# Performance work log

Measured on AMD Instinct MI355X. Metric: run time of the kernel, lower is better.

## Reference

```python
import jax, jax.numpy as jnp
import numpy as np

B, N, FD, H = 8, 256, 1024, 256
RATIO, TEMP = 0.6, 0.5


def setup_inputs() -> dict:
    key = jax.random.key(0)
    ks = jax.random.split(key, 5)
    x = jax.random.normal(ks[0], (B, N, FD), dtype=jnp.float32)
    s1 = 1.0 / np.sqrt(2 * FD)
    W1 = jax.random.uniform(ks[1], (H, 2 * FD), minval=-s1, maxval=s1, dtype=jnp.float32)
    b1 = jax.random.uniform(ks[2], (H,), minval=-s1, maxval=s1, dtype=jnp.float32)
    s2 = 1.0 / np.sqrt(H)
    W2 = jax.random.uniform(ks[3], (1, H), minval=-s2, maxval=s2, dtype=jnp.float32)
    b2 = jax.random.uniform(ks[4], (1,), minval=-s2, maxval=s2, dtype=jnp.float32)
    return {"x": x, "W1": W1, "b1": b1, "W2": W2, "b2": b2}


def reference(x, W1, b1, W2, b2):
    Bb, Nn, Fd = x.shape
    # Linear on cat([row, col]) == row @ W1[:, :F].T + col @ W1[:, F:].T + b1,
    # so project nodes once and broadcast-add instead of materializing [N,N,2F].
    pr = jnp.einsum('bnf,hf->bnh', x, W1[:, :Fd])  # row projections
    pc = jnp.einsum('bnf,hf->bnh', x, W1[:, Fd:])  # col projections
    h = jax.nn.relu(pr[:, :, None, :] + pc[:, None, :, :] + b1)  # [B,N,N,H]
    edge_scores = jnp.einsum('bijh,h->bij', h, W2[0]) + b2[0]    # [B,N,N]
    flat = edge_scores.reshape(Bb, Nn * Nn)
    soft_mask = jax.nn.softmax(flat / TEMP, axis=1)
    k = int(RATIO * Nn * Nn)
    topk_vals, _ = jax.lax.top_k(soft_mask, k)
    threshold = topk_vals[:, -1:]
    causal_mask = jnp.where(soft_mask >= threshold, soft_mask, jnp.zeros_like(soft_mask))
    causal_mask = causal_mask / (causal_mask.sum(axis=1, keepdims=True) + 1e-12)
    conf_mask = 1.0 - causal_mask
    causal_adj = causal_mask.reshape(Bb, Nn, Nn)
    conf_adj = conf_mask.reshape(Bb, Nn, Nn)
    return (causal_adj, conf_adj, edge_scores, soft_mask)
```

## Files before the change

### kernel.cpp

```cpp
#include <hip/hip_runtime.h>

#define BB 8
#define NN 256
#define FDIM 1024
#define HDIM 256
#define NSQ 65536
#define ROWS 2048
#define KSEL 39321
#define NBIN 16384

typedef short s16x8 __attribute__((ext_vector_type(8)));
typedef float f32x4 __attribute__((ext_vector_type(4)));

__device__ __forceinline__ unsigned fkey(float f) {
  unsigned u = __float_as_uint(f);
  return (u & 0x80000000u) ? ~u : (u | 0x80000000u);
}
__device__ __forceinline__ float finv(unsigned k) {
  unsigned u = (k & 0x80000000u) ? (k & 0x7fffffffu) : ~k;
  return __uint_as_float(u);
}
__device__ __forceinline__ unsigned short f2bf(float f) {
  unsigned u = __float_as_uint(f);
  unsigned r = (u + 0x7fffu + ((u >> 16) & 1u)) >> 16;
  return (unsigned short)r;
}

__global__ __launch_bounds__(256) void k_prep(const float* __restrict__ X,
                                              const float* __restrict__ W1,
                                              unsigned short* __restrict__ XB,
                                              unsigned short* __restrict__ W1B,
                                              unsigned* __restrict__ zero) {
  const int bx = blockIdx.x, t = threadIdx.x;
  if (bx < 1280) {
    const float* src = (bx < 1024) ? X : W1;
    unsigned short* dst = (bx < 1024) ? XB : W1B;
    const int idx = ((bx < 1024 ? bx : bx - 1024) * 256 + t) * 8;
    float4 v0 = *(const float4*)&src[idx];
    float4 v1 = *(const float4*)&src[idx + 4];
    s16x8 o;
    o[0] = (short)f2bf(v0.x); o[1] = (short)f2bf(v0.y); o[2] = (short)f2bf(v0.z); o[3] = (short)f2bf(v0.w);
    o[4] = (short)f2bf(v1.x); o[5] = (short)f2bf(v1.y); o[6] = (short)f2bf(v1.z); o[7] = (short)f2bf(v1.w);
    *(s16x8*)&dst[idx] = o;
  } else {
    const int idx = ((bx - 1280) * 256 + t) * 4;
    *(uint4*)&zero[idx] = make_uint4(0u, 0u, 0u, 0u);
  }
}

#define LDSW 72
__global__ __launch_bounds__(256) void k_gemm(const unsigned short* __restrict__ XB,
                                              const unsigned short* __restrict__ W1B,
                                              const float* __restrict__ b1,
                                              float* __restrict__ PRBT,
                                              float* __restrict__ PCT) {
  const int bm = blockIdx.x * 64;
  const int bn = blockIdx.y * 64;
  const int t = threadIdx.x;
  __shared__ short As[64 * LDSW];
  __shared__ short Bs[64 * LDSW];
  const int sr = t >> 2, cg = t & 3;
  const unsigned short* pa = XB + (bm + sr) * FDIM + cg * 16;
  const unsigned short* pb = (bn < 256)
      ? (W1B + (bn + sr) * (2 * FDIM) + cg * 16)
      : (W1B + (bn - 256 + sr) * (2 * FDIM) + FDIM + cg * 16);
  const int w = t >> 6, lane = t & 63;
  const int wm = (w >> 1) * 32, wn = (w & 1) * 32;
  const int q = lane >> 4, m16 = lane & 15;
  f32x4 acc[2][2] = {};
  for (int k0 = 0; k0 < FDIM; k0 += 64) {
    s16x8 a0 = *(const s16x8*)(pa + k0);
    s16x8 a1 = *(const s16x8*)(pa + k0 + 8);
    s16x8 b0 = *(const s16x8*)(pb + k0);
    s16x8 b1v = *(const s16x8*)(pb + k0 + 8);
    __syncthreads();
    *(s16x8*)&As[sr * LDSW + cg * 16]     = a0;
    *(s16x8*)&As[sr * LDSW + cg * 16 + 8] = a1;
    *(s16x8*)&Bs[sr * LDSW + cg * 16]     = b0;
    *(s16x8*)&Bs[sr * LDSW + cg * 16 + 8] = b1v;
    __syncthreads();
    {
      s16x8 af0 = *(s16x8*)&As[(wm + m16) * LDSW + q * 8];
      s16x8 af1 = *(s16x8*)&As[(wm + 16 + m16) * LDSW + q * 8];
      s16x8 bf0 = *(s16x8*)&Bs[(wn + m16) * LDSW + q * 8];
      s16x8 bf1 = *(s16x8*)&Bs[(wn + 16 + m16) * LDSW + q * 8];
      acc[0][0] = __builtin_amdgcn_mfma_f32_16x16x32_bf16(af0, bf0, acc[0][0], 0, 0, 0);
      acc[0][1] = __builtin_amdgcn_mfma_f32_16x16x32_bf16(af0, bf1, acc[0][1], 0, 0, 0);
      acc[1][0] = __builtin_amdgcn_mfma_f32_16x16x32_bf16(af1, bf0, acc[1][0], 0, 0, 0);
      acc[1][1] = __builtin_amdgcn_mfma_f32_16x16x32_bf16(af1, bf1, acc[1][1], 0, 0, 0);
    }
    {
      s16x8 af0 = *(s16x8*)&As[(wm + m16) * LDSW + 32 + q * 8];
      s16x8 af1 = *(s16x8*)&As[(wm + 16 + m16) * LDSW + 32 + q * 8];
      s16x8 bf0 = *(s16x8*)&Bs[(wn + m16) * LDSW + 32 + q * 8];
      s16x8 bf1 = *(s16x8*)&Bs[(wn + 16 + m16) * LDSW + 32 + q * 8];
      acc[0][0] = __builtin_amdgcn_mfma_f32_16x16x32_bf16(af0, bf0, acc[0][0], 0, 0, 0);
      acc[0][1] = __builtin_amdgcn_mfma_f32_16x16x32_bf16(af0, bf1, acc[0][1], 0, 0, 0);
      acc[1][0] = __builtin_amdgcn_mfma_f32_16x16x32_bf16(af1, bf0, acc[1][0], 0, 0, 0);
      acc[1][1] = __builtin_amdgcn_mfma_f32_16x16x32_bf16(af1, bf1, acc[1][1], 0, 0, 0);
    }
  }
#pragma unroll
  for (int rt = 0; rt < 2; ++rt) {
#pragma unroll
    for (int ct = 0; ct < 2; ++ct) {
      const int hn = bn + wn + ct * 16 + m16;
      const int row0 = bm + wm + rt * 16 + q * 4;
      if (hn < 256) {
        const float bias = b1[hn];
        float4 v = make_float4(acc[rt][ct][0] + bias, acc[rt][ct][1] + bias,
                               acc[rt][ct][2] + bias, acc[rt][ct][3] + bias);
        *(float4*)&PRBT[hn * ROWS + row0] = v;
      } else {
        float4 v = make_float4(acc[rt][ct][0], acc[rt][ct][1],
                               acc[rt][ct][2], acc[rt][ct][3]);
        *(float4*)&PCT[(hn - 256) * ROWS + row0] = v;
      }
    }
  }
}

__global__ __launch_bounds__(256) void k_edge(const float* __restrict__ PRBT,
                                              const float* __restrict__ PCT,
                                              const float* __restrict__ W2,
                                              const float* __restrict__ b2,
                                              float* __restrict__ edge,
                                              unsigned* __restrict__ gcount,
                                              float* __restrict__ gvsum) {
  const int b = blockIdx.z;
  const int i0 = blockIdx.y * 64, j0 = blockIdx.x * 32;
  const int t = threadIdx.x;
  __shared__ float prs[64][68];
  __shared__ float pcs[64][36];
  __shared__ float w2s[HDIM];
  __shared__ unsigned lhc[NBIN / 2];
  __shared__ float lhv[NBIN];
  w2s[t] = W2[t];
#pragma unroll
  for (int i = 0; i < 8; ++i) ((uint4*)lhc)[t + i * 256] = make_uint4(0u, 0u, 0u, 0u);
#pragma unroll
  for (int i = 0; i < 16; ++i) ((float4*)lhv)[t + i * 256] = make_float4(0.f, 0.f, 0.f, 0.f);
  const float bias = b2[0];
  const int tmi = t >> 4, tnj = t & 15;
  float acc[4][2] = {};
  for (int h0 = 0; h0 < HDIM; h0 += 64) {
    __syncthreads();
#pragma unroll
    for (int it = 0; it < 4; ++it) {
      int hh = it * 16 + (t >> 4);
      int ig = t & 15;
      *(float4*)&prs[hh][ig * 4] =
          *(const float4*)&PRBT[(h0 + hh) * ROWS + b * NN + i0 + ig * 4];
    }
#pragma unroll
    for (int it = 0; it < 2; ++it) {
      int hh = it * 32 + (t >> 3);
      int jg = t & 7;
      *(float4*)&pcs[hh][jg * 4] =
          *(const float4*)&PCT[(h0 + hh) * ROWS + b * NN + j0 + jg * 4];
    }
    __syncthreads();
#pragma unroll 8
    for (int h = 0; h < 64; ++h) {
      const float w = w2s[h0 + h];
      const float4 a = *(const float4*)&prs[h][tmi * 4];
      const float2 c = *(const float2*)&pcs[h][tnj * 2];
      const float ai[4] = {a.x, a.y, a.z, a.w};
#pragma unroll
      for (int i = 0; i < 4; ++i) {
        acc[i][0] += fmaxf(ai[i] + c.x, 0.f) * w;
        acc[i][1] += fmaxf(ai[i] + c.y, 0.f) * w;
      }
    }
  }
  const int ibase = i0 + tmi * 4, jbase = j0 + tnj * 2;
#pragma unroll
  for (int i = 0; i < 4; ++i) {
    float2 v = make_float2(acc[i][0] + bias, acc[i][1] + bias);
    *(float2*)&edge[b * NSQ + (ibase + i) * NN + jbase] = v;
    float ex = __expf(v.x * 2.f), ey = __expf(v.y * 2.f);
    unsigned bx = fkey(v.x) >> 18, by = fkey(v.y) >> 18;
    atomicAdd(&lhc[bx >> 1], 1u << ((bx & 1) * 16));
    atomicAdd(&lhv[bx], ex);
    atomicAdd(&lhc[by >> 1], 1u << ((by & 1) * 16));
    atomicAdd(&lhv[by], ey);
  }
  __syncthreads();
  unsigned* gc = gcount + b * NBIN;
  float* gv = gvsum + b * NBIN;
#pragma unroll
  for (int i = 0; i < 32; ++i) {
    const int idx = t + i * 256;
    unsigned wv = lhc[idx];
    if (wv) {
      unsigned lo = wv & 0xFFFFu, hi = wv >> 16;
      if (lo) atomicAdd(&gc[2 * idx], lo);
      if (hi) atomicAdd(&gc[2 * idx + 1], hi);
    }
  }
#pragma unroll
  for (int i = 0; i < 64; ++i) {
    const int idx = t + i * 256;
    float vv = lhv[idx];
    if (vv != 0.f) atomicAdd(&gv[idx], vv);
  }
}

__global__ __launch_bounds__(256) void k_out(const float* __restrict__ edge,
                                             const unsigned* __restrict__ gcount,
                                             const float* __restrict__ gvsum,
                                             float* __restrict__ soft,
                                             float* __restrict__ causal,
                                             float* __restrict__ conf) {
  const int b = blockIdx.y;
  const int t = threadIdx.x;
  __shared__ unsigned S[256];
  __shared__ float V[256];
  __shared__ unsigned ou[1];
  __shared__ float of[3];
  const unsigned* hc = gcount + b * NBIN;
  const float* hv = gvsum + b * NBIN;
  unsigned cs = 0; float vs = 0.f;
  for (int i = 0; i < 64; ++i) { cs += hc[t * 64 + i]; vs += hv[t * 64 + i]; }
  S[t] = cs; V[t] = vs;
  __syncthreads();
  for (int off = 1; off < 256; off <<= 1) {
    unsigned su = (t + off < 256) ? S[t + off] : 0u;
    float vu = (t + off < 256) ? V[t + off] : 0.f;
    __syncthreads();
    S[t] += su; V[t] += vu;
    __syncthreads();
  }
  if (t == 0) of[2] = V[0];
  const int above = (int)(S[t] - cs);
  if (above < KSEL && (int)S[t] >= KSEL) {
    int cum = above;
    float vcum = V[t] - vs;
    for (int i = 63; i >= 0; --i) {
      unsigned c = hc[t * 64 + i];
      float v = hv[t * 64 + i];
      cum += (int)c;
      if (cum >= KSEL) { ou[0] = (unsigned)(t * 64 + i); of[0] = vcum; of[1] = v; break; }
      vcum += v;
    }
  }
  __syncthreads();
  const float th = finv(ou[0] << 18);
  const float Z = of[2];
  const float invZ = 1.f / Z;
  const float msum = (of[0] + of[1]) * invZ;
  const float invD = 1.f / (msum + 1e-12f);
  const int off = b * NSQ + blockIdx.x * 2048 + t * 8;
#pragma unroll
  for (int i = 0; i < 8; i += 4) {
    float4 v = *(const float4*)&edge[off + i];
    float4 o = make_float4(__expf(v.x * 2.f) * invZ, __expf(v.y * 2.f) * invZ,
                           __expf(v.z * 2.f) * invZ, __expf(v.w * 2.f) * invZ);
    *(float4*)&soft[off + i] = o;
    float cx = v.x >= th ? o.x * invD : 0.f;
    float cy = v.y >= th ? o.y * invD : 0.f;
    float cz = v.z >= th ? o.z * invD : 0.f;
    float cw = v.w >= th ? o.w * invD : 0.f;
    *(float4*)&causal[off + i] = make_float4(cx, cy, cz, cw);
    *(float4*)&conf[off + i]   = make_float4(1.f - cx, 1.f - cy, 1.f - cz, 1.f - cw);
  }
}

extern "C" void kernel_launch(void* const* d_in, const int* in_sizes, int n_in,
                              void* d_out, int out_size, void* d_ws, size_t ws_size,
                              hipStream_t stream) {
  const float* x  = (const float*)d_in[0];
  const float* W1 = (const float*)d_in[1];
  const float* b1 = (const float*)d_in[2];
  const float* W2 = (const float*)d_in[3];
  const float* b2 = (const float*)d_in[4];

  float* out = (float*)d_out;
  float* causal = out;
  float* conf   = out + 1 * 524288;
  float* edge   = out + 2 * 524288;
  float* soft   = out + 3 * 524288;

  float* ws = (float*)d_ws;
  float*          PRBT   = ws;
  float*          PCT    = ws + 524288;
  unsigned short* XB     = (unsigned short*)(ws + 1048576);
  unsigned short* W1B    = (unsigned short*)(ws + 2097152);
  unsigned*       gcount = (unsigned*)(ws + 2359296);
  float*          gvsum  = (float*)(ws + 2490368);

  k_prep<<<1536, 256, 0, stream>>>(x, W1, XB, W1B, gcount);
  k_gemm<<<dim3(32, 8), 256, 0, stream>>>(XB, W1B, b1, PRBT, PCT);
  k_edge<<<dim3(8, 4, 8), 256, 0, stream>>>(PRBT, PCT, W2, b2, edge, gcount, gvsum);
  k_out<<<dim3(32, 8), 256, 0, stream>>>(edge, gcount, gvsum, soft, causal, conf);
}
```

Before: 120.4 us.

## Halve histogram bins, double k_edge threads, prefetch GEMM tiles in registers

The top-k histogram shrinks from 16384 to 8192 bins per batch by dropping one more mantissa bit from the sort key. This cuts the LDS footprint and the cost of zeroing and flushing the histogram in k_edge and of scanning it in k_out. k_edge now runs 512 threads per block, each computing a 2x2 output micro-tile instead of 4x2, so each of the 256 blocks has more waves to hide latency. The GEMM loads the next K-slice into registers before the current one is consumed. The risk is that the coarser bins make the top-k threshold cruder, so more elements near it could be misclassified.

```diff
diff --git a/kernel.cpp b/kernel.cpp
--- a/kernel.cpp
+++ b/kernel.cpp
@@ -7,7 +7,7 @@
 #define NSQ 65536
 #define ROWS 2048
 #define KSEL 39321
-#define NBIN 16384
+#define NBIN 8192
 
 typedef short s16x8 __attribute__((ext_vector_type(8)));
 typedef float f32x4 __attribute__((ext_vector_type(4)));
@@ -68,16 +68,22 @@
   const int wm = (w >> 1) * 32, wn = (w & 1) * 32;
   const int q = lane >> 4, m16 = lane & 15;
   f32x4 acc[2][2] = {};
+  s16x8 ra0 = *(const s16x8*)(pa);
+  s16x8 ra1 = *(const s16x8*)(pa + 8);
+  s16x8 rb0 = *(const s16x8*)(pb);
+  s16x8 rb1 = *(const s16x8*)(pb + 8);
   for (int k0 = 0; k0 < FDIM; k0 += 64) {
-    s16x8 a0 = *(const s16x8*)(pa + k0);
-    s16x8 a1 = *(const s16x8*)(pa + k0 + 8);
-    s16x8 b0 = *(const s16x8*)(pb + k0);
-    s16x8 b1v = *(const s16x8*)(pb + k0 + 8);
-    __syncthreads();
-    *(s16x8*)&As[sr * LDSW + cg * 16]     = a0;
-    *(s16x8*)&As[sr * LDSW + cg * 16 + 8] = a1;
-    *(s16x8*)&Bs[sr * LDSW + cg * 16]     = b0;
-    *(s16x8*)&Bs[sr * LDSW + cg * 16 + 8] = b1v;
+    __syncthreads();
+    *(s16x8*)&As[sr * LDSW + cg * 16]     = ra0;
+    *(s16x8*)&As[sr * LDSW + cg * 16 + 8] = ra1;
+    *(s16x8*)&Bs[sr * LDSW + cg * 16]     = rb0;
+    *(s16x8*)&Bs[sr * LDSW + cg * 16 + 8] = rb1;
+    if (k0 + 64 < FDIM) {
+      ra0 = *(const s16x8*)(pa + k0 + 64);
+      ra1 = *(const s16x8*)(pa + k0 + 72);
+      rb0 = *(const s16x8*)(pb + k0 + 64);
+      rb1 = *(const s16x8*)(pb + k0 + 72);
+    }
     __syncthreads();
     {
       s16x8 af0 = *(s16x8*)&As[(wm + m16) * LDSW + q * 8];
@@ -120,7 +126,7 @@
   }
 }
 
-__global__ __launch_bounds__(256) void k_edge(const float* __restrict__ PRBT,
+__global__ __launch_bounds__(512) void k_edge(const float* __restrict__ PRBT,
                                               const float* __restrict__ PCT,
                                               const float* __restrict__ W2,
                                               const float* __restrict__ b2,
@@ -135,27 +141,25 @@
   __shared__ float w2s[HDIM];
   __shared__ unsigned lhc[NBIN / 2];
   __shared__ float lhv[NBIN];
-  w2s[t] = W2[t];
-#pragma unroll
-  for (int i = 0; i < 8; ++i) ((uint4*)lhc)[t + i * 256] = make_uint4(0u, 0u, 0u, 0u);
-#pragma unroll
-  for (int i = 0; i < 16; ++i) ((float4*)lhv)[t + i * 256] = make_float4(0.f, 0.f, 0.f, 0.f);
+  if (t < HDIM) w2s[t] = W2[t];
+#pragma unroll
+  for (int i = 0; i < 2; ++i) ((uint4*)lhc)[t + i * 512] = make_uint4(0u, 0u, 0u, 0u);
+#pragma unroll
+  for (int i = 0; i < 4; ++i) ((float4*)lhv)[t + i * 512] = make_float4(0.f, 0.f, 0.f, 0.f);
   const float bias = b2[0];
   const int tmi = t >> 4, tnj = t & 15;
-  float acc[4][2] = {};
+  float acc[2][2] = {};
   for (int h0 = 0; h0 < HDIM; h0 += 64) {
     __syncthreads();
 #pragma unroll
-    for (int it = 0; it < 4; ++it) {
-      int hh = it * 16 + (t >> 4);
-      int ig = t & 15;
+    for (int s = 0; s < 2; ++s) {
+      int idx = t + s * 512;
+      int hh = idx >> 4, ig = idx & 15;
       *(float4*)&prs[hh][ig * 4] =
           *(const float4*)&PRBT[(h0 + hh) * ROWS + b * NN + i0 + ig * 4];
     }
-#pragma unroll
-    for (int it = 0; it < 2; ++it) {
-      int hh = it * 32 + (t >> 3);
-      int jg = t & 7;
+    {
+      int hh = t >> 3, jg = t & 7;
       *(float4*)&pcs[hh][jg * 4] =
           *(const float4*)&PCT[(h0 + hh) * ROWS + b * NN + j0 + jg * 4];
     }
@@ -163,23 +167,21 @@
 #pragma unroll 8
     for (int h = 0; h < 64; ++h) {
       const float w = w2s[h0 + h];
-      const float4 a = *(const float4*)&prs[h][tmi * 4];
+      const float2 a = *(const float2*)&prs[h][tmi * 2];
       const float2 c = *(const float2*)&pcs[h][tnj * 2];
-      const float ai[4] = {a.x, a.y, a.z, a.w};
-#pragma unroll
-      for (int i = 0; i < 4; ++i) {
-        acc[i][0] += fmaxf(ai[i] + c.x, 0.f) * w;
-        acc[i][1] += fmaxf(ai[i] + c.y, 0.f) * w;
-      }
-    }
-  }
-  const int ibase = i0 + tmi * 4, jbase = j0 + tnj * 2;
-#pragma unroll
-  for (int i = 0; i < 4; ++i) {
+      acc[0][0] += fmaxf(a.x + c.x, 0.f) * w;
+      acc[0][1] += fmaxf(a.x + c.y, 0.f) * w;
+      acc[1][0] += fmaxf(a.y + c.x, 0.f) * w;
+      acc[1][1] += fmaxf(a.y + c.y, 0.f) * w;
+    }
+  }
+  const int ibase = i0 + tmi * 2, jbase = j0 + tnj * 2;
+#pragma unroll
+  for (int i = 0; i < 2; ++i) {
     float2 v = make_float2(acc[i][0] + bias, acc[i][1] + bias);
     *(float2*)&edge[b * NSQ + (ibase + i) * NN + jbase] = v;
     float ex = __expf(v.x * 2.f), ey = __expf(v.y * 2.f);
-    unsigned bx = fkey(v.x) >> 18, by = fkey(v.y) >> 18;
+    unsigned bx = fkey(v.x) >> 19, by = fkey(v.y) >> 19;
     atomicAdd(&lhc[bx >> 1], 1u << ((bx & 1) * 16));
     atomicAdd(&lhv[bx], ex);
     atomicAdd(&lhc[by >> 1], 1u << ((by & 1) * 16));
@@ -189,8 +191,8 @@
   unsigned* gc = gcount + b * NBIN;
   float* gv = gvsum + b * NBIN;
 #pragma unroll
-  for (int i = 0; i < 32; ++i) {
-    const int idx = t + i * 256;
+  for (int i = 0; i < 8; ++i) {
+    const int idx = t + i * 512;
     unsigned wv = lhc[idx];
     if (wv) {
       unsigned lo = wv & 0xFFFFu, hi = wv >> 16;
@@ -199,8 +201,8 @@
     }
   }
 #pragma unroll
-  for (int i = 0; i < 64; ++i) {
-    const int idx = t + i * 256;
+  for (int i = 0; i < 16; ++i) {
+    const int idx = t + i * 512;
     float vv = lhv[idx];
     if (vv != 0.f) atomicAdd(&gv[idx], vv);
   }
@@ -221,7 +223,7 @@
   const unsigned* hc = gcount + b * NBIN;
   const float* hv = gvsum + b * NBIN;
   unsigned cs = 0; float vs = 0.f;
-  for (int i = 0; i < 64; ++i) { cs += hc[t * 64 + i]; vs += hv[t * 64 + i]; }
+  for (int i = 0; i < 32; ++i) { cs += hc[t * 32 + i]; vs += hv[t * 32 + i]; }
   S[t] = cs; V[t] = vs;
   __syncthreads();
   for (int off = 1; off < 256; off <<= 1) {
@@ -236,16 +238,16 @@
   if (above < KSEL && (int)S[t] >= KSEL) {
     int cum = above;
     float vcum = V[t] - vs;
-    for (int i = 63; i >= 0; --i) {
-      unsigned c = hc[t * 64 + i];
-      float v = hv[t * 64 + i];
+    for (int i = 31; i >= 0; --i) {
+      unsigned c = hc[t * 32 + i];
+      float v = hv[t * 32 + i];
       cum += (int)c;
-      if (cum >= KSEL) { ou[0] = (unsigned)(t * 64 + i); of[0] = vcum; of[1] = v; break; }
+      if (cum >= KSEL) { ou[0] = (unsigned)(t * 32 + i); of[0] = vcum; of[1] = v; break; }
       vcum += v;
     }
   }
   __syncthreads();
-  const float th = finv(ou[0] << 18);
+  const float th = finv(ou[0] << 19);
   const float Z = of[2];
   const float invZ = 1.f / Z;
   const float msum = (of[0] + of[1]) * invZ;
@@ -287,10 +289,10 @@
   unsigned short* XB     = (unsigned short*)(ws + 1048576);
   unsigned short* W1B    = (unsigned short*)(ws + 2097152);
   unsigned*       gcount = (unsigned*)(ws + 2359296);
-  float*          gvsum  = (float*)(ws + 2490368);
-
-  k_prep<<<1536, 256, 0, stream>>>(x, W1, XB, W1B, gcount);
+  float*          gvsum  = (float*)(ws + 2424832);
+
+  k_prep<<<1408, 256, 0, stream>>>(x, W1, XB, W1B, gcount);
   k_gemm<<<dim3(32, 8), 256, 0, stream>>>(XB, W1B, b1, PRBT, PCT);
-  k_edge<<<dim3(8, 4, 8), 256, 0, stream>>>(PRBT, PCT, W2, b2, edge, gcount, gvsum);
+  k_edge<<<dim3(8, 4, 8), 512, 0, stream>>>(PRBT, PCT, W2, b2, edge, gcount, gvsum);
   k_out<<<dim3(32, 8), 256, 0, stream>>>(edge, gcount, gvsum, soft, causal, conf);
 }
```

Result: faster. 106.5 us (-11.5%).
